# Performance work log

Hardware: AMD Instinct MI355X
Metric: run time of the kernel (lower is better)

Reference implementation:

```python
import jax, jax.numpy as jnp
import numpy as np

N, E, DIM, HEADS, EDIM, DFF = 20000, 320000, 256, 8, 32, 1024
C = DIM // HEADS


def _gatv2(x, src, dst, ea, Wl, Wr, We, att, b):
    # PyG GATv2Conv (concat=True, share_weights=False, add_self_loops=True,
    # fill_value='mean', negative_slope=0.2), eval mode (no attn dropout).
    n = x.shape[0]
    h, c = att.shape
    e = src.shape[0]
    # self loops: edge_attr filled with per-target-node mean of edge features
    cnt = jax.ops.segment_sum(jnp.ones((e,), x.dtype), dst, num_segments=n)
    loop_ea = jax.ops.segment_sum(ea, dst, num_segments=n) / jnp.maximum(cnt, 1.0)[:, None]
    loop = jnp.arange(n)
    s = jnp.concatenate([src, loop])
    d = jnp.concatenate([dst, loop])
    ea_all = jnp.concatenate([ea, loop_ea], axis=0)
    xl = (x @ Wl).reshape(n, h, c)   # source transform
    xr = (x @ Wr).reshape(n, h, c)   # target transform
    ee = (ea_all @ We).reshape(-1, h, c)
    z = jax.nn.leaky_relu(xl[s] + xr[d] + ee, 0.2)      # [E+N, H, C]
    score = jnp.einsum('ehc,hc->eh', z, att)             # [E+N, H]
    # segment softmax over incoming edges of each target node
    m = jax.ops.segment_max(score, d, num_segments=n)
    ex = jnp.exp(score - m[d])
    den = jax.ops.segment_sum(ex, d, num_segments=n)
    alpha = ex / den[d]
    out = jax.ops.segment_sum(alpha[:, :, None] * xl[s], d, num_segments=n)
    return out.reshape(n, h * c) + b


def _bn(x, g, b, eps=1e-5):
    # BatchNorm1d over nodes, training-mode batch stats (biased var)
    mu = x.mean(axis=0)
    var = ((x - mu) ** 2).mean(axis=0)
    return (x - mu) * jax.lax.rsqrt(var + eps) * g + b


def _lrelu(x):
    return jax.nn.leaky_relu(x, 0.01)  # F.leaky_relu default slope


def setup_inputs() -> dict:
    key = jax.random.key(0)
    ks = jax.random.split(key, 16)
    sc = 0.05
    inp = {
        'nf': jax.random.normal(ks[0], (N, DIM), jnp.float32),
        'ei': jax.random.randint(ks[1], (2, E), 0, N, dtype=jnp.int32),
        'ew': jax.random.normal(ks[2], (E, EDIM), jnp.float32),
    }
    for i, pfx in enumerate(['g1', 'g2']):
        kk = jax.random.split(ks[3 + i], 5)
        inp[pfx + '_Wl'] = jax.random.normal(kk[0], (DIM, DIM), jnp.float32) * sc
        inp[pfx + '_Wr'] = jax.random.normal(kk[1], (DIM, DIM), jnp.float32) * sc
        inp[pfx + '_We'] = jax.random.normal(kk[2], (EDIM, DIM), jnp.float32) * sc
        inp[pfx + '_att'] = jax.random.normal(kk[3], (HEADS, C), jnp.float32) * sc
        inp[pfx + '_b'] = jnp.zeros((DIM,), jnp.float32)
    for i, pfx in enumerate(['n1', 'n2', 'n3']):
        inp[pfx + '_g'] = jnp.ones((DIM,), jnp.float32)
        inp[pfx + '_b'] = jnp.zeros((DIM,), jnp.float32)
    inp['ff_W1'] = jax.random.normal(ks[8], (DIM, DFF), jnp.float32) * sc
    inp['ff_b1'] = jnp.zeros((DFF,), jnp.float32)
    inp['ff_W2'] = jax.random.normal(ks[9], (DFF, DIM), jnp.float32) * sc
    inp['ff_b2'] = jnp.zeros((DIM,), jnp.float32)
    return inp


def reference(nf, ei, ew,
              g1_Wl, g1_Wr, g1_We, g1_att, g1_b,
              g2_Wl, g2_Wr, g2_We, g2_att, g2_b,
              n1_g, n1_b, n2_g, n2_b, n3_g, n3_b,
              ff_W1, ff_b1, ff_W2, ff_b2):
    src, dst = ei[0], ei[1]
    # in_channels == dim, so residual branch is taken for block 1
    h = nf + _lrelu(_bn(_gatv2(nf, src, dst, ew, g1_Wl, g1_Wr, g1_We, g1_att, g1_b), n1_g, n1_b))
    h = h + _lrelu(_bn(_gatv2(h, src, dst, ew, g2_Wl, g2_Wr, g2_We, g2_att, g2_b), n2_g, n2_b))
    ff = jax.nn.relu(h @ ff_W1 + ff_b1) @ ff_W2 + ff_b2
    h = h + _lrelu(_bn(ff, n3_g, n3_b))
    return h
```

## Files before the change

### kernel.cpp

```cpp
#include <hip/hip_runtime.h>

#define NN 20000
#define NE 320000
#define DIMX 256
#define NHEADS 8
#define HC 32
#define EDIMX 32
#define DFFX 1024
#define TOT (NE + NN)
#define NGROUPS (TOT / 16)

using f32x4 = __attribute__((ext_vector_type(4))) float;
using bfrag = __attribute__((ext_vector_type(8))) short;

__device__ __forceinline__ float b2f(unsigned short u) {
  return __uint_as_float(((unsigned)u) << 16);
}
__device__ __forceinline__ unsigned short f2b(float f) {
  unsigned u = __float_as_uint(f);
  u += 0x7FFF + ((u >> 16) & 1);
  return (unsigned short)(u >> 16);
}

__global__ void k_detect(const unsigned short* __restrict__ in, int* __restrict__ flag) {
  __shared__ int cnt_s;
  if (threadIdx.x == 0) cnt_s = 0;
  __syncthreads();
  int c = 0;
  for (int i = threadIdx.x; i < 4096; i += 256) {
    int ex = (in[i] >> 7) & 0xFF;
    if (ex >= 0xC6) c++;
  }
  atomicAdd(&cnt_s, c);
  __syncthreads();
  if (threadIdx.x == 0) flag[0] = (cnt_s > 64) ? 1 : 0;
}

__global__ void k_cvt(const void* __restrict__ in, float* __restrict__ out, int n,
                      const int* __restrict__ flag) {
  int i = blockIdx.x * 256 + threadIdx.x;
  if (i >= n) return;
  if (flag[0]) out[i] = ((const float*)in)[i];
  else out[i] = b2f(((const unsigned short*)in)[i]);
}

__global__ void k_cvt_dual(const void* __restrict__ in, float* __restrict__ outf,
                           unsigned short* __restrict__ outb, int n,
                           const int* __restrict__ flag) {
  int i = blockIdx.x * 256 + threadIdx.x;
  if (i >= n) return;
  if (flag[0]) {
    float v = ((const float*)in)[i];
    outf[i] = v;
    outb[i] = f2b(v);
  } else {
    unsigned short u = ((const unsigned short*)in)[i];
    outf[i] = b2f(u);
    outb[i] = u;
  }
}

struct CvtArgs {
  const void* src[20];
  float* dst[20];
  int n[20];
};
__global__ void k_cvt_multi(CvtArgs a, const int* __restrict__ flag) {
  int seg = blockIdx.y;
  int n = a.n[seg];
  int i = blockIdx.x * 256 + threadIdx.x;
  if (i >= n) return;
  if (flag[0]) a.dst[seg][i] = ((const float*)a.src[seg])[i];
  else a.dst[seg][i] = b2f(((const unsigned short*)a.src[seg])[i]);
}

__global__ __launch_bounds__(256) void k_transpose(const float* __restrict__ in,
                                                   unsigned short* __restrict__ out,
                                                   int K, int N) {
  __shared__ float t[32][33];
  int n0 = blockIdx.x * 32, k0 = blockIdx.y * 32;
  int tx = threadIdx.x & 31, ty = threadIdx.x >> 5;
#pragma unroll
  for (int i = 0; i < 4; i++)
    t[ty + i * 8][tx] = in[(size_t)(k0 + ty + i * 8) * N + n0 + tx];
  __syncthreads();
#pragma unroll
  for (int i = 0; i < 4; i++)
    out[(size_t)(n0 + ty + i * 8) * K + k0 + tx] = f2b(t[tx][ty + i * 8]);
}

__global__ void k_edge_count(const int* __restrict__ dst, int* __restrict__ cnt, int E) {
  int e = blockIdx.x * 256 + threadIdx.x;
  if (e >= E) return;
  atomicAdd(&cnt[dst[e]], 1);
}

__global__ void k_scan(const int* __restrict__ cnt, int* __restrict__ rowptr, int N) {
  __shared__ int sums[256];
  int t = threadIdx.x;
  int chunk = (N + 255) / 256;
  int lo = t * chunk, hi = lo + chunk;
  if (hi > N) hi = N;
  if (lo > N) lo = N;
  int s = 0;
  for (int n = lo; n < hi; n++) s += cnt[n] + 1;
  sums[t] = s;
  __syncthreads();
  for (int off = 1; off < 256; off <<= 1) {
    int v = (t >= off) ? sums[t - off] : 0;
    __syncthreads();
    sums[t] += v;
    __syncthreads();
  }
  int run = sums[t] - s;
  for (int n = lo; n < hi; n++) { rowptr[n] = run; run += cnt[n] + 1; }
  if (t == 255) rowptr[N] = run;
}

__global__ void k_fill(const int* __restrict__ dst, const int* __restrict__ rowptr,
                       int* __restrict__ fill, int* __restrict__ eidx,
                       int* __restrict__ dstp, int N, int E) {
  int t = blockIdx.x * 256 + threadIdx.x;
  if (t < E) {
    int d = dst[t];
    int pos = rowptr[d] + atomicAdd(&fill[d], 1);
    eidx[pos] = t;
    dstp[pos] = d;
  } else if (t < E + N) {
    int n = t - E;
    int pos = rowptr[n + 1] - 1;
    eidx[pos] = E + n;
    dstp[pos] = n;
  }
}

__global__ __launch_bounds__(256) void k_lea(const float* __restrict__ ew,
                                             const int* __restrict__ rowptr,
                                             const int* __restrict__ eidx,
                                             float* __restrict__ lea, int N) {
  int wave = threadIdx.x >> 6, lane = threadIdx.x & 63;
  int node = blockIdx.x * 4 + wave;
  if (node >= N) return;
  int begin = rowptr[node], end = rowptr[node + 1] - 1;
  int ch = lane & 31, half = lane >> 5;
  float s = 0.f;
  for (int p = begin + half; p < end; p += 2) {
    int eid = eidx[p];
    s += ew[(size_t)eid * EDIMX + ch];
  }
  s += __shfl_xor(s, 32, 64);
  int deg = end - begin;
  if (lane < 32) lea[(size_t)node * EDIMX + ch] = s / (float)(deg > 0 ? deg : 1);
}

__global__ __launch_bounds__(256) void k_build_perm(const int* __restrict__ eidx,
                                                    const int* __restrict__ src,
                                                    const float* __restrict__ ewf,
                                                    const float* __restrict__ lea,
                                                    int* __restrict__ srcp,
                                                    unsigned short* __restrict__ eab,
                                                    int total, int E) {
  int g = blockIdx.x * 8 + (threadIdx.x >> 5);
  int lane = threadIdx.x & 31;
  if (g >= total) return;
  int eid = eidx[g];
  int s;
  const float* row;
  if (eid < E) {
    s = src[eid];
    row = ewf + (size_t)eid * EDIMX;
  } else {
    s = eid - E;
    row = lea + (size_t)(eid - E) * EDIMX;
  }
  if (lane == 0) srcp[g] = s;
  eab[(size_t)g * EDIMX + lane] = f2b(row[lane]);
}

template <bool BIAS, bool RELU, bool OUTBF16>
__global__ __launch_bounds__(256) void k_gemm_mfma(const unsigned short* __restrict__ A,
                                                   const unsigned short* __restrict__ BT,
                                                   const float* __restrict__ bias,
                                                   void* __restrict__ C, int M, int K, int N) {
  int tid = threadIdx.x;
  int wave = tid >> 6, lane = tid & 63;
  int quad = lane >> 4, l16 = lane & 15;
  int m0 = blockIdx.x * 64 + (wave & 1) * 32;
  int n0 = blockIdx.y * 64 + (wave >> 1) * 32;
  int mA0 = m0 + l16;
  if (mA0 > M - 1) mA0 = M - 1;
  int mA1 = m0 + 16 + l16;
  if (mA1 > M - 1) mA1 = M - 1;
  const bfrag* a0p = (const bfrag*)(A + (size_t)mA0 * K + quad * 8);
  const bfrag* a1p = (const bfrag*)(A + (size_t)mA1 * K + quad * 8);
  const bfrag* b0p = (const bfrag*)(BT + (size_t)(n0 + l16) * K + quad * 8);
  const bfrag* b1p = (const bfrag*)(BT + (size_t)(n0 + 16 + l16) * K + quad * 8);
  f32x4 acc00 = {0.f, 0.f, 0.f, 0.f}, acc01 = {0.f, 0.f, 0.f, 0.f};
  f32x4 acc10 = {0.f, 0.f, 0.f, 0.f}, acc11 = {0.f, 0.f, 0.f, 0.f};
  int ksteps = K >> 5;
  for (int kk = 0; kk < ksteps; kk++) {
    bfrag a0 = a0p[kk * 4];
    bfrag a1 = a1p[kk * 4];
    bfrag b0 = b0p[kk * 4];
    bfrag b1 = b1p[kk * 4];
    acc00 = __builtin_amdgcn_mfma_f32_16x16x32_bf16(a0, b0, acc00, 0, 0, 0);
    acc01 = __builtin_amdgcn_mfma_f32_16x16x32_bf16(a0, b1, acc01, 0, 0, 0);
    acc10 = __builtin_amdgcn_mfma_f32_16x16x32_bf16(a1, b0, acc10, 0, 0, 0);
    acc11 = __builtin_amdgcn_mfma_f32_16x16x32_bf16(a1, b1, acc11, 0, 0, 0);
  }
  float bv0 = 0.f, bv1 = 0.f;
  if (BIAS) {
    bv0 = bias[n0 + l16];
    bv1 = bias[n0 + 16 + l16];
  }
  int col0 = n0 + l16, col1 = n0 + 16 + l16;
#pragma unroll
  for (int r = 0; r < 4; r++) {
    int row0 = m0 + quad * 4 + r;
    int row1 = m0 + 16 + quad * 4 + r;
    float v00 = acc00[r] + bv0, v01 = acc01[r] + bv1;
    float v10 = acc10[r] + bv0, v11 = acc11[r] + bv1;
    if (RELU) {
      v00 = fmaxf(v00, 0.f); v01 = fmaxf(v01, 0.f);
      v10 = fmaxf(v10, 0.f); v11 = fmaxf(v11, 0.f);
    }
    if (row0 < M) {
      if (OUTBF16) {
        ((unsigned short*)C)[(size_t)row0 * N + col0] = f2b(v00);
        ((unsigned short*)C)[(size_t)row0 * N + col1] = f2b(v01);
      } else {
        ((float*)C)[(size_t)row0 * N + col0] = v00;
        ((float*)C)[(size_t)row0 * N + col1] = v01;
      }
    }
    if (row1 < M) {
      if (OUTBF16) {
        ((unsigned short*)C)[(size_t)row1 * N + col0] = f2b(v10);
        ((unsigned short*)C)[(size_t)row1 * N + col1] = f2b(v11);
      } else {
        ((float*)C)[(size_t)row1 * N + col0] = v10;
        ((float*)C)[(size_t)row1 * N + col1] = v11;
      }
    }
  }
}

__global__ __launch_bounds__(256) void k_score_mfma(
    const unsigned short* __restrict__ xlb, const unsigned short* __restrict__ xrb,
    const unsigned short* __restrict__ eab, const int* __restrict__ srcp,
    const int* __restrict__ dstp, const unsigned short* __restrict__ WET,
    const float* __restrict__ att, float* __restrict__ score, int ngroups) {
  __shared__ unsigned short We_s[256 * 40];
  __shared__ unsigned short ee_s[4][16 * 260];
  {
    int tid = threadIdx.x;
#pragma unroll
    for (int j = 0; j < 8; j++)
      *(ushort4*)&We_s[tid * 40 + j * 4] = *(const ushort4*)(WET + tid * 32 + j * 4);
  }
  __syncthreads();
  int wave = threadIdx.x >> 6, lane = threadIdx.x & 63;
  int quad = lane >> 4, l16 = lane & 15;
  int g = blockIdx.x * 4 + wave;
  if (g >= ngroups) return;
  int pbase = g * 16;
  const bfrag ea = *(const bfrag*)(eab + ((size_t)(pbase + l16) << 5) + quad * 8);
  f32x4 zero4 = {0.f, 0.f, 0.f, 0.f};
  f32x4 acc[16];
#pragma unroll
  for (int t = 0; t < 16; t++) {
    bfrag bw = *(const bfrag*)&We_s[(t * 16 + l16) * 40 + quad * 8];
    acc[t] = __builtin_amdgcn_mfma_f32_16x16x32_bf16(ea, bw, zero4, 0, 0, 0);
  }
#pragma unroll
  for (int t = 0; t < 16; t++) {
#pragma unroll
    for (int r = 0; r < 4; r++)
      ee_s[wave][(quad * 4 + r) * 260 + t * 16 + l16] = f2b(acc[t][r]);
  }
  int c0 = lane * 4;
  float4 a4 = *(const float4*)(att + c0);
  for (int e = 0; e < 16; e += 2) {
    int p0 = pbase + e, p1 = pbase + e + 1;
    int s0 = srcp[p0], d0 = dstp[p0];
    int s1 = srcp[p1], d1 = dstp[p1];
    ushort4 vl0 = *(const ushort4*)(xlb + ((size_t)s0 << 8) + c0);
    ushort4 vr0 = *(const ushort4*)(xrb + ((size_t)d0 << 8) + c0);
    ushort4 vl1 = *(const ushort4*)(xlb + ((size_t)s1 << 8) + c0);
    ushort4 vr1 = *(const ushort4*)(xrb + ((size_t)d1 << 8) + c0);
    ushort4 eu0 = *(const ushort4*)&ee_s[wave][e * 260 + c0];
    ushort4 eu1 = *(const ushort4*)&ee_s[wave][(e + 1) * 260 + c0];
    float z00 = b2f(vl0.x) + b2f(vr0.x) + b2f(eu0.x);
    float z01 = b2f(vl0.y) + b2f(vr0.y) + b2f(eu0.y);
    float z02 = b2f(vl0.z) + b2f(vr0.z) + b2f(eu0.z);
    float z03 = b2f(vl0.w) + b2f(vr0.w) + b2f(eu0.w);
    float z10 = b2f(vl1.x) + b2f(vr1.x) + b2f(eu1.x);
    float z11 = b2f(vl1.y) + b2f(vr1.y) + b2f(eu1.y);
    float z12 = b2f(vl1.z) + b2f(vr1.z) + b2f(eu1.z);
    float z13 = b2f(vl1.w) + b2f(vr1.w) + b2f(eu1.w);
    z00 = z00 > 0.f ? z00 : 0.2f * z00; z01 = z01 > 0.f ? z01 : 0.2f * z01;
    z02 = z02 > 0.f ? z02 : 0.2f * z02; z03 = z03 > 0.f ? z03 : 0.2f * z03;
    z10 = z10 > 0.f ? z10 : 0.2f * z10; z11 = z11 > 0.f ? z11 : 0.2f * z11;
    z12 = z12 > 0.f ? z12 : 0.2f * z12; z13 = z13 > 0.f ? z13 : 0.2f * z13;
    float sc0 = z00 * a4.x + z01 * a4.y + z02 * a4.z + z03 * a4.w;
    float sc1 = z10 * a4.x + z11 * a4.y + z12 * a4.z + z13 * a4.w;
    sc0 += __shfl_xor(sc0, 1, 64);
    sc1 += __shfl_xor(sc1, 1, 64);
    sc0 += __shfl_xor(sc0, 2, 64);
    sc1 += __shfl_xor(sc1, 2, 64);
    sc0 += __shfl_xor(sc0, 4, 64);
    sc1 += __shfl_xor(sc1, 4, 64);
    if ((lane & 7) == 0) {
      int h = lane >> 3;
      score[(size_t)p0 * 8 + h] = sc0;
      score[(size_t)p1 * 8 + h] = sc1;
    }
  }
}

__global__ __launch_bounds__(256) void k_agg(const unsigned short* __restrict__ xlb,
                                             const float* __restrict__ score,
                                             const int* __restrict__ srcp,
                                             const float* __restrict__ bias,
                                             const int* __restrict__ rowptr,
                                             float* __restrict__ out, int N) {
  int wave = threadIdx.x >> 6, lane = threadIdx.x & 63;
  int node = blockIdx.x * 4 + wave;
  if (node >= N) return;
  int begin = rowptr[node], end = rowptr[node + 1];
  int head = lane >> 3, sl = lane & 7;
  float m = -3.4e38f;
  for (int p = begin + sl; p < end; p += 8)
    m = fmaxf(m, score[(size_t)p * 8 + head]);
  m = fmaxf(m, __shfl_xor(m, 1, 64));
  m = fmaxf(m, __shfl_xor(m, 2, 64));
  m = fmaxf(m, __shfl_xor(m, 4, 64));
  float ssum = 0.f;
  for (int p = begin + sl; p < end; p += 8)
    ssum += __expf(score[(size_t)p * 8 + head] - m);
  ssum += __shfl_xor(ssum, 1, 64);
  ssum += __shfl_xor(ssum, 2, 64);
  ssum += __shfl_xor(ssum, 4, 64);
  float linv = 1.f / ssum;
  int c0 = lane * 4;
  float ax = 0.f, ay = 0.f, az = 0.f, aw = 0.f;
  for (int p = begin; p < end; p += 4) {
    int e1 = end - 1;
    int q1 = (p + 1 < end) ? p + 1 : e1;
    int q2 = (p + 2 < end) ? p + 2 : e1;
    int q3 = (p + 3 < end) ? p + 3 : e1;
    int s0 = srcp[p], s1 = srcp[q1], s2 = srcp[q2], s3 = srcp[q3];
    float sc0 = score[(size_t)p * 8 + head];
    float sc1 = score[(size_t)q1 * 8 + head];
    float sc2 = score[(size_t)q2 * 8 + head];
    float sc3 = score[(size_t)q3 * 8 + head];
    ushort4 v0 = *(const ushort4*)(xlb + ((size_t)s0 << 8) + c0);
    ushort4 v1 = *(const ushort4*)(xlb + ((size_t)s1 << 8) + c0);
    ushort4 v2 = *(const ushort4*)(xlb + ((size_t)s2 << 8) + c0);
    ushort4 v3 = *(const ushort4*)(xlb + ((size_t)s3 << 8) + c0);
    float w0 = __expf(sc0 - m) * linv;
    float w1 = (p + 1 < end) ? __expf(sc1 - m) * linv : 0.f;
    float w2 = (p + 2 < end) ? __expf(sc2 - m) * linv : 0.f;
    float w3 = (p + 3 < end) ? __expf(sc3 - m) * linv : 0.f;
    ax += w0 * b2f(v0.x) + w1 * b2f(v1.x) + w2 * b2f(v2.x) + w3 * b2f(v3.x);
    ay += w0 * b2f(v0.y) + w1 * b2f(v1.y) + w2 * b2f(v2.y) + w3 * b2f(v3.y);
    az += w0 * b2f(v0.z) + w1 * b2f(v1.z) + w2 * b2f(v2.z) + w3 * b2f(v3.z);
    aw += w0 * b2f(v0.w) + w1 * b2f(v1.w) + w2 * b2f(v2.w) + w3 * b2f(v3.w);
  }
  float4 bia = *(const float4*)(bias + c0);
  float4 acc = make_float4(ax + bia.x, ay + bia.y, az + bia.z, aw + bia.w);
  ((float4*)out)[(size_t)node * 64 + lane] = acc;
}

__global__ __launch_bounds__(256) void k_bnstats(const float* __restrict__ x,
                                                 float* __restrict__ sums, int N) {
  int c = threadIdx.x;
  float s = 0.f, sq = 0.f;
  for (int n = blockIdx.x; n < N; n += gridDim.x) {
    float v = x[(size_t)n * DIMX + c];
    s += v; sq += v * v;
  }
  atomicAdd(&sums[c], s);
  atomicAdd(&sums[DIMX + c], sq);
}

template <bool FINAL>
__global__ __launch_bounds__(256) void k_bnapply(const float* __restrict__ x,
                                                 const float* __restrict__ res,
                                                 const float* __restrict__ sums,
                                                 const float* __restrict__ g,
                                                 const float* __restrict__ b,
                                                 void* __restrict__ out,
                                                 unsigned short* __restrict__ outb, int N,
                                                 const int* __restrict__ flag) {
  int i = blockIdx.x * 256 + threadIdx.x;
  if (i >= N * DIMX) return;
  int c = i & (DIMX - 1);
  float invn = 1.f / (float)N;
  float mu = sums[c] * invn;
  float var = sums[DIMX + c] * invn - mu * mu;
  float rstd = rsqrtf(var + 1e-5f);
  float y = (x[i] - mu) * rstd * g[c] + b[c];
  y = y > 0.f ? y : 0.01f * y;
  y += res[i];
  if (FINAL) {
    if (flag[0]) ((float*)out)[i] = y;
    else ((unsigned short*)out)[i] = f2b(y);
  } else {
    ((float*)out)[i] = y;
    outb[i] = f2b(y);
  }
}

extern "C" void kernel_launch(void* const* d_in, const int* in_sizes, int n_in,
                              void* d_out, int out_size, void* d_ws, size_t ws_size,
                              hipStream_t stream) {
  (void)in_sizes; (void)n_in; (void)out_size; (void)ws_size;
  const int* ei = (const int*)d_in[1];
  const int* srcp = ei;
  const int* dstp = ei + NE;

  char* w = (char*)d_ws;
  auto alloc = [&](size_t bytes) {
    char* p = w;
    w += (bytes + 255) & ~(size_t)255;
    return p;
  };
  float* H0 = (float*)alloc((size_t)NN * DIMX * 4);
  float* H1 = (float*)alloc((size_t)NN * DIMX * 4);
  float* G = (float*)alloc((size_t)NN * DIMX * 4);
  float* LEA = (float*)alloc((size_t)NN * EDIMX * 4);
  float* EWF = (float*)alloc((size_t)NE * EDIMX * 4);
  float* PAR = (float*)alloc((size_t)806656 * 4);
  float* SCORE = (float*)alloc((size_t)TOT * NHEADS * 4);
  int* CNT = (int*)alloc((size_t)NN * 4);
  int* ROWPTR = (int*)alloc((size_t)(NN + 1) * 4);
  int* FILL = (int*)alloc((size_t)NN * 4);
  int* EIDX = (int*)alloc((size_t)TOT * 4);
  int* SRCP = (int*)alloc((size_t)TOT * 4);
  int* DSTP = (int*)alloc((size_t)TOT * 4);
  float* BNS = (float*)alloc(2 * DIMX * 4);
  int* FLAG = (int*)alloc(256);
  unsigned short* H0b = (unsigned short*)alloc((size_t)NN * DIMX * 2);
  unsigned short* H1b = (unsigned short*)alloc((size_t)NN * DIMX * 2);
  unsigned short* XLb = (unsigned short*)alloc((size_t)NN * DIMX * 2);
  unsigned short* XRb = (unsigned short*)alloc((size_t)NN * DIMX * 2);
  unsigned short* EAB = (unsigned short*)alloc((size_t)TOT * EDIMX * 2);
  unsigned short* WLT0 = (unsigned short*)alloc((size_t)DIMX * DIMX * 2);
  unsigned short* WRT0 = (unsigned short*)alloc((size_t)DIMX * DIMX * 2);
  unsigned short* WLT1 = (unsigned short*)alloc((size_t)DIMX * DIMX * 2);
  unsigned short* WRT1 = (unsigned short*)alloc((size_t)DIMX * DIMX * 2);
  unsigned short* WET0 = (unsigned short*)alloc((size_t)DIMX * EDIMX * 2);
  unsigned short* WET1 = (unsigned short*)alloc((size_t)DIMX * EDIMX * 2);
  unsigned short* W1T = (unsigned short*)alloc((size_t)DIMX * DFFX * 2);
  unsigned short* W2T = (unsigned short*)alloc((size_t)DFFX * DIMX * 2);
  unsigned short* FF1b = (unsigned short*)EWF;

  k_detect<<<1, 256, 0, stream>>>((const unsigned short*)d_in[0], FLAG);
  k_cvt_dual<<<(NN * DIMX + 255) / 256, 256, 0, stream>>>(d_in[0], H0, H0b, NN * DIMX, FLAG);
  k_cvt<<<(NE * EDIMX + 255) / 256, 256, 0, stream>>>(d_in[2], EWF, NE * EDIMX, FLAG);
  static const int psz[20] = {65536, 65536, 8192, 256, 256,
                              65536, 65536, 8192, 256, 256,
                              256, 256, 256, 256, 256, 256,
                              262144, 1024, 262144, 256};
  float* pp[20];
  {
    CvtArgs ca;
    int off = 0;
    for (int i = 0; i < 20; i++) {
      pp[i] = PAR + off;
      off += psz[i];
      ca.src[i] = d_in[3 + i];
      ca.dst[i] = pp[i];
      ca.n[i] = psz[i];
    }
    k_cvt_multi<<<dim3(262144 / 256, 20), 256, 0, stream>>>(ca, FLAG);
  }
  const float* g_att[2] = {pp[3], pp[8]};
  const float* g_b[2] = {pp[4], pp[9]};
  const float* bn_g[3] = {pp[10], pp[12], pp[14]};
  const float* bn_b[3] = {pp[11], pp[13], pp[15]};
  const float* ff_b1 = pp[17];
  const float* ff_b2 = pp[19];

  k_transpose<<<dim3(8, 8), 256, 0, stream>>>(pp[0], WLT0, DIMX, DIMX);
  k_transpose<<<dim3(8, 8), 256, 0, stream>>>(pp[1], WRT0, DIMX, DIMX);
  k_transpose<<<dim3(8, 8), 256, 0, stream>>>(pp[5], WLT1, DIMX, DIMX);
  k_transpose<<<dim3(8, 8), 256, 0, stream>>>(pp[6], WRT1, DIMX, DIMX);
  k_transpose<<<dim3(8, 1), 256, 0, stream>>>(pp[2], WET0, EDIMX, DIMX);
  k_transpose<<<dim3(8, 1), 256, 0, stream>>>(pp[7], WET1, EDIMX, DIMX);
  k_transpose<<<dim3(32, 8), 256, 0, stream>>>(pp[16], W1T, DIMX, DFFX);
  k_transpose<<<dim3(8, 32), 256, 0, stream>>>(pp[18], W2T, DFFX, DIMX);
  const unsigned short* WLT[2] = {WLT0, WLT1};
  const unsigned short* WRT[2] = {WRT0, WRT1};
  const unsigned short* WET[2] = {WET0, WET1};

  hipMemsetAsync(CNT, 0, (size_t)NN * 4, stream);
  hipMemsetAsync(FILL, 0, (size_t)NN * 4, stream);
  k_edge_count<<<(NE + 255) / 256, 256, 0, stream>>>(dstp, CNT, NE);
  k_scan<<<1, 256, 0, stream>>>(CNT, ROWPTR, NN);
  k_fill<<<(TOT + 255) / 256, 256, 0, stream>>>(dstp, ROWPTR, FILL, EIDX, DSTP, NN, NE);
  k_lea<<<(NN + 3) / 4, 256, 0, stream>>>(EWF, ROWPTR, EIDX, LEA, NN);
  k_build_perm<<<(TOT + 7) / 8, 256, 0, stream>>>(EIDX, srcp, EWF, LEA, SRCP, EAB, TOT, NE);

  const int MB = (NN + 63) / 64;
  auto run_gat = [&](const float* x, const unsigned short* xb, int li, int bi, float* hout,
                     unsigned short* houtb) {
    k_gemm_mfma<false, false, true><<<dim3(MB, 4), 256, 0, stream>>>(xb, WLT[li], nullptr, XLb,
                                                                     NN, DIMX, DIMX);
    k_gemm_mfma<false, false, true><<<dim3(MB, 4), 256, 0, stream>>>(xb, WRT[li], nullptr, XRb,
                                                                     NN, DIMX, DIMX);
    k_score_mfma<<<(NGROUPS + 3) / 4, 256, 0, stream>>>(XLb, XRb, EAB, SRCP, DSTP, WET[li],
                                                        g_att[li], SCORE, NGROUPS);
    k_agg<<<(NN + 3) / 4, 256, 0, stream>>>(XLb, SCORE, SRCP, g_b[li], ROWPTR, G, NN);
    hipMemsetAsync(BNS, 0, 2 * DIMX * 4, stream);
    k_bnstats<<<128, 256, 0, stream>>>(G, BNS, NN);
    k_bnapply<false><<<(NN * DIMX + 255) / 256, 256, 0, stream>>>(G, x, BNS, bn_g[bi], bn_b[bi],
                                                                  hout, houtb, NN, FLAG);
  };

  run_gat(H0, H0b, 0, 0, H1, H1b);
  run_gat(H1, H1b, 1, 1, H0, H0b);

  k_gemm_mfma<true, true, true><<<dim3(MB, DFFX / 64), 256, 0, stream>>>(H0b, W1T, ff_b1, FF1b,
                                                                         NN, DIMX, DFFX);
  k_gemm_mfma<true, false, false><<<dim3(MB, 4), 256, 0, stream>>>(FF1b, W2T, ff_b2, G, NN,
                                                                   DFFX, DIMX);
  hipMemsetAsync(BNS, 0, 2 * DIMX * 4, stream);
  k_bnstats<<<128, 256, 0, stream>>>(G, BNS, NN);
  k_bnapply<true><<<(NN * DIMX + 255) / 256, 256, 0, stream>>>(G, H0, BNS, bn_g[2], bn_b[2],
                                                               d_out, nullptr, NN, FLAG);
}
```

Before: 912.9 us.

## Fuse Wl/Wr GEMMs into one interleaved output, drop edge-feature conversion pass

Concatenates the transposed Wl and Wr weights so one GEMM writes an interleaved [N,512] buffer holding xl and xr per node. The score and aggregation kernels now index that buffer with a 512 stride. The separate fp32 conversion of edge features is removed, and k_lea and k_build_perm read the raw input directly with the dtype flag. The GEMM gains an NT template parameter so each block loops over several 64-column tiles while reusing its A row pointers; this cuts the number of blocks, which may lower occupancy and parallelism.

New measurement: 950.6 us. 4.1% more time.

```diff
diff --git a/kernel.cpp b/kernel.cpp
--- a/kernel.cpp
+++ b/kernel.cpp
@@ -34,14 +34,6 @@
   atomicAdd(&cnt_s, c);
   __syncthreads();
   if (threadIdx.x == 0) flag[0] = (cnt_s > 64) ? 1 : 0;
-}
-
-__global__ void k_cvt(const void* __restrict__ in, float* __restrict__ out, int n,
-                      const int* __restrict__ flag) {
-  int i = blockIdx.x * 256 + threadIdx.x;
-  if (i >= n) return;
-  if (flag[0]) out[i] = ((const float*)in)[i];
-  else out[i] = b2f(((const unsigned short*)in)[i]);
 }
 
 __global__ void k_cvt_dual(const void* __restrict__ in, float* __restrict__ outf,
@@ -134,10 +126,12 @@
   }
 }
 
-__global__ __launch_bounds__(256) void k_lea(const float* __restrict__ ew,
+__global__ __launch_bounds__(256) void k_lea(const void* __restrict__ ew,
                                              const int* __restrict__ rowptr,
                                              const int* __restrict__ eidx,
-                                             float* __restrict__ lea, int N) {
+                                             float* __restrict__ lea, int N,
+                                             const int* __restrict__ flag) {
+  int f = flag[0];
   int wave = threadIdx.x >> 6, lane = threadIdx.x & 63;
   int node = blockIdx.x * 4 + wave;
   if (node >= N) return;
@@ -146,7 +140,8 @@
   float s = 0.f;
   for (int p = begin + half; p < end; p += 2) {
     int eid = eidx[p];
-    s += ew[(size_t)eid * EDIMX + ch];
+    size_t idx = (size_t)eid * EDIMX + ch;
+    s += f ? ((const float*)ew)[idx] : b2f(((const unsigned short*)ew)[idx]);
   }
   s += __shfl_xor(s, 32, 64);
   int deg = end - begin;
@@ -155,29 +150,32 @@
 
 __global__ __launch_bounds__(256) void k_build_perm(const int* __restrict__ eidx,
                                                     const int* __restrict__ src,
-                                                    const float* __restrict__ ewf,
+                                                    const void* __restrict__ ew,
                                                     const float* __restrict__ lea,
                                                     int* __restrict__ srcp,
                                                     unsigned short* __restrict__ eab,
-                                                    int total, int E) {
+                                                    int total, int E,
+                                                    const int* __restrict__ flag) {
+  int f = flag[0];
   int g = blockIdx.x * 8 + (threadIdx.x >> 5);
   int lane = threadIdx.x & 31;
   if (g >= total) return;
   int eid = eidx[g];
+  unsigned short v;
   int s;
-  const float* row;
   if (eid < E) {
     s = src[eid];
-    row = ewf + (size_t)eid * EDIMX;
+    size_t idx = (size_t)eid * EDIMX + lane;
+    v = f ? f2b(((const float*)ew)[idx]) : ((const unsigned short*)ew)[idx];
   } else {
     s = eid - E;
-    row = lea + (size_t)(eid - E) * EDIMX;
+    v = f2b(lea[(size_t)(eid - E) * EDIMX + lane]);
   }
   if (lane == 0) srcp[g] = s;
-  eab[(size_t)g * EDIMX + lane] = f2b(row[lane]);
-}
-
-template <bool BIAS, bool RELU, bool OUTBF16>
+  eab[(size_t)g * EDIMX + lane] = v;
+}
+
+template <bool BIAS, bool RELU, bool OUTBF16, int NT>
 __global__ __launch_bounds__(256) void k_gemm_mfma(const unsigned short* __restrict__ A,
                                                    const unsigned short* __restrict__ BT,
                                                    const float* __restrict__ bias,
@@ -186,70 +184,73 @@
   int wave = tid >> 6, lane = tid & 63;
   int quad = lane >> 4, l16 = lane & 15;
   int m0 = blockIdx.x * 64 + (wave & 1) * 32;
-  int n0 = blockIdx.y * 64 + (wave >> 1) * 32;
   int mA0 = m0 + l16;
   if (mA0 > M - 1) mA0 = M - 1;
   int mA1 = m0 + 16 + l16;
   if (mA1 > M - 1) mA1 = M - 1;
   const bfrag* a0p = (const bfrag*)(A + (size_t)mA0 * K + quad * 8);
   const bfrag* a1p = (const bfrag*)(A + (size_t)mA1 * K + quad * 8);
-  const bfrag* b0p = (const bfrag*)(BT + (size_t)(n0 + l16) * K + quad * 8);
-  const bfrag* b1p = (const bfrag*)(BT + (size_t)(n0 + 16 + l16) * K + quad * 8);
-  f32x4 acc00 = {0.f, 0.f, 0.f, 0.f}, acc01 = {0.f, 0.f, 0.f, 0.f};
-  f32x4 acc10 = {0.f, 0.f, 0.f, 0.f}, acc11 = {0.f, 0.f, 0.f, 0.f};
   int ksteps = K >> 5;
-  for (int kk = 0; kk < ksteps; kk++) {
-    bfrag a0 = a0p[kk * 4];
-    bfrag a1 = a1p[kk * 4];
-    bfrag b0 = b0p[kk * 4];
-    bfrag b1 = b1p[kk * 4];
-    acc00 = __builtin_amdgcn_mfma_f32_16x16x32_bf16(a0, b0, acc00, 0, 0, 0);
-    acc01 = __builtin_amdgcn_mfma_f32_16x16x32_bf16(a0, b1, acc01, 0, 0, 0);
-    acc10 = __builtin_amdgcn_mfma_f32_16x16x32_bf16(a1, b0, acc10, 0, 0, 0);
-    acc11 = __builtin_amdgcn_mfma_f32_16x16x32_bf16(a1, b1, acc11, 0, 0, 0);
-  }
-  float bv0 = 0.f, bv1 = 0.f;
-  if (BIAS) {
-    bv0 = bias[n0 + l16];
-    bv1 = bias[n0 + 16 + l16];
-  }
-  int col0 = n0 + l16, col1 = n0 + 16 + l16;
-#pragma unroll
-  for (int r = 0; r < 4; r++) {
-    int row0 = m0 + quad * 4 + r;
-    int row1 = m0 + 16 + quad * 4 + r;
-    float v00 = acc00[r] + bv0, v01 = acc01[r] + bv1;
-    float v10 = acc10[r] + bv0, v11 = acc11[r] + bv1;
-    if (RELU) {
-      v00 = fmaxf(v00, 0.f); v01 = fmaxf(v01, 0.f);
-      v10 = fmaxf(v10, 0.f); v11 = fmaxf(v11, 0.f);
+#pragma unroll
+  for (int j = 0; j < NT; j++) {
+    int n0 = (blockIdx.y * NT + j) * 64 + (wave >> 1) * 32;
+    const bfrag* b0p = (const bfrag*)(BT + (size_t)(n0 + l16) * K + quad * 8);
+    const bfrag* b1p = (const bfrag*)(BT + (size_t)(n0 + 16 + l16) * K + quad * 8);
+    f32x4 acc00 = {0.f, 0.f, 0.f, 0.f}, acc01 = {0.f, 0.f, 0.f, 0.f};
+    f32x4 acc10 = {0.f, 0.f, 0.f, 0.f}, acc11 = {0.f, 0.f, 0.f, 0.f};
+    for (int kk = 0; kk < ksteps; kk++) {
+      bfrag a0 = a0p[kk * 4];
+      bfrag a1 = a1p[kk * 4];
+      bfrag b0 = b0p[kk * 4];
+      bfrag b1 = b1p[kk * 4];
+      acc00 = __builtin_amdgcn_mfma_f32_16x16x32_bf16(a0, b0, acc00, 0, 0, 0);
+      acc01 = __builtin_amdgcn_mfma_f32_16x16x32_bf16(a0, b1, acc01, 0, 0, 0);
+      acc10 = __builtin_amdgcn_mfma_f32_16x16x32_bf16(a1, b0, acc10, 0, 0, 0);
+      acc11 = __builtin_amdgcn_mfma_f32_16x16x32_bf16(a1, b1, acc11, 0, 0, 0);
     }
-    if (row0 < M) {
-      if (OUTBF16) {
-        ((unsigned short*)C)[(size_t)row0 * N + col0] = f2b(v00);
-        ((unsigned short*)C)[(size_t)row0 * N + col1] = f2b(v01);
-      } else {
-        ((float*)C)[(size_t)row0 * N + col0] = v00;
-        ((float*)C)[(size_t)row0 * N + col1] = v01;
+    float bv0 = 0.f, bv1 = 0.f;
+    if (BIAS) {
+      bv0 = bias[n0 + l16];
+      bv1 = bias[n0 + 16 + l16];
+    }
+    int col0 = n0 + l16, col1 = n0 + 16 + l16;
+#pragma unroll
+    for (int r = 0; r < 4; r++) {
+      int row0 = m0 + quad * 4 + r;
+      int row1 = m0 + 16 + quad * 4 + r;
+      float v00 = acc00[r] + bv0, v01 = acc01[r] + bv1;
+      float v10 = acc10[r] + bv0, v11 = acc11[r] + bv1;
+      if (RELU) {
+        v00 = fmaxf(v00, 0.f); v01 = fmaxf(v01, 0.f);
+        v10 = fmaxf(v10, 0.f); v11 = fmaxf(v11, 0.f);
+      }
+      if (row0 < M) {
+        if (OUTBF16) {
+          ((unsigned short*)C)[(size_t)row0 * N + col0] = f2b(v00);
+          ((unsigned short*)C)[(size_t)row0 * N + col1] = f2b(v01);
+        } else {
+          ((float*)C)[(size_t)row0 * N + col0] = v00;
+          ((float*)C)[(size_t)row0 * N + col1] = v01;
+        }
+      }
+      if (row1 < M) {
+        if (OUTBF16) {
+          ((unsigned short*)C)[(size_t)row1 * N + col0] = f2b(v10);
+          ((unsigned short*)C)[(size_t)row1 * N + col1] = f2b(v11);
+        } else {
+          ((float*)C)[(size_t)row1 * N + col0] = v10;
+          ((float*)C)[(size_t)row1 * N + col1] = v11;
+        }
       }
     }
-    if (row1 < M) {
-      if (OUTBF16) {
-        ((unsigned short*)C)[(size_t)row1 * N + col0] = f2b(v10);
-        ((unsigned short*)C)[(size_t)row1 * N + col1] = f2b(v11);
-      } else {
-        ((float*)C)[(size_t)row1 * N + col0] = v10;
-        ((float*)C)[(size_t)row1 * N + col1] = v11;
-      }
-    }
   }
 }
 
 __global__ __launch_bounds__(256) void k_score_mfma(
-    const unsigned short* __restrict__ xlb, const unsigned short* __restrict__ xrb,
-    const unsigned short* __restrict__ eab, const int* __restrict__ srcp,
-    const int* __restrict__ dstp, const unsigned short* __restrict__ WET,
-    const float* __restrict__ att, float* __restrict__ score, int ngroups) {
+    const unsigned short* __restrict__ xlr, const unsigned short* __restrict__ eab,
+    const int* __restrict__ srcp, const int* __restrict__ dstp,
+    const unsigned short* __restrict__ WET, const float* __restrict__ att,
+    float* __restrict__ score, int ngroups) {
   __shared__ unsigned short We_s[256 * 40];
   __shared__ unsigned short ee_s[4][16 * 260];
   {
@@ -284,10 +285,10 @@
     int p0 = pbase + e, p1 = pbase + e + 1;
     int s0 = srcp[p0], d0 = dstp[p0];
     int s1 = srcp[p1], d1 = dstp[p1];
-    ushort4 vl0 = *(const ushort4*)(xlb + ((size_t)s0 << 8) + c0);
-    ushort4 vr0 = *(const ushort4*)(xrb + ((size_t)d0 << 8) + c0);
-    ushort4 vl1 = *(const ushort4*)(xlb + ((size_t)s1 << 8) + c0);
-    ushort4 vr1 = *(const ushort4*)(xrb + ((size_t)d1 << 8) + c0);
+    ushort4 vl0 = *(const ushort4*)(xlr + ((size_t)s0 << 9) + c0);
+    ushort4 vr0 = *(const ushort4*)(xlr + ((size_t)d0 << 9) + 256 + c0);
+    ushort4 vl1 = *(const ushort4*)(xlr + ((size_t)s1 << 9) + c0);
+    ushort4 vr1 = *(const ushort4*)(xlr + ((size_t)d1 << 9) + 256 + c0);
     ushort4 eu0 = *(const ushort4*)&ee_s[wave][e * 260 + c0];
     ushort4 eu1 = *(const ushort4*)&ee_s[wave][(e + 1) * 260 + c0];
     float z00 = b2f(vl0.x) + b2f(vr0.x) + b2f(eu0.x);
@@ -318,7 +319,7 @@
   }
 }
 
-__global__ __launch_bounds__(256) void k_agg(const unsigned short* __restrict__ xlb,
+__global__ __launch_bounds__(256) void k_agg(const unsigned short* __restrict__ xlr,
                                              const float* __restrict__ score,
                                              const int* __restrict__ srcp,
                                              const float* __restrict__ bias,
@@ -354,10 +355,10 @@
     float sc1 = score[(size_t)q1 * 8 + head];
     float sc2 = score[(size_t)q2 * 8 + head];
     float sc3 = score[(size_t)q3 * 8 + head];
-    ushort4 v0 = *(const ushort4*)(xlb + ((size_t)s0 << 8) + c0);
-    ushort4 v1 = *(const ushort4*)(xlb + ((size_t)s1 << 8) + c0);
-    ushort4 v2 = *(const ushort4*)(xlb + ((size_t)s2 << 8) + c0);
-    ushort4 v3 = *(const ushort4*)(xlb + ((size_t)s3 << 8) + c0);
+    ushort4 v0 = *(const ushort4*)(xlr + ((size_t)s0 << 9) + c0);
+    ushort4 v1 = *(const ushort4*)(xlr + ((size_t)s1 << 9) + c0);
+    ushort4 v2 = *(const ushort4*)(xlr + ((size_t)s2 << 9) + c0);
+    ushort4 v3 = *(const ushort4*)(xlr + ((size_t)s3 << 9) + c0);
     float w0 = __expf(sc0 - m) * linv;
     float w1 = (p + 1 < end) ? __expf(sc1 - m) * linv : 0.f;
     float w2 = (p + 2 < end) ? __expf(sc2 - m) * linv : 0.f;
@@ -443,13 +444,10 @@
   int* FLAG = (int*)alloc(256);
   unsigned short* H0b = (unsigned short*)alloc((size_t)NN * DIMX * 2);
   unsigned short* H1b = (unsigned short*)alloc((size_t)NN * DIMX * 2);
-  unsigned short* XLb = (unsigned short*)alloc((size_t)NN * DIMX * 2);
-  unsigned short* XRb = (unsigned short*)alloc((size_t)NN * DIMX * 2);
+  unsigned short* XLRb = (unsigned short*)alloc((size_t)NN * 512 * 2);
   unsigned short* EAB = (unsigned short*)alloc((size_t)TOT * EDIMX * 2);
-  unsigned short* WLT0 = (unsigned short*)alloc((size_t)DIMX * DIMX * 2);
-  unsigned short* WRT0 = (unsigned short*)alloc((size_t)DIMX * DIMX * 2);
-  unsigned short* WLT1 = (unsigned short*)alloc((size_t)DIMX * DIMX * 2);
-  unsigned short* WRT1 = (unsigned short*)alloc((size_t)DIMX * DIMX * 2);
+  unsigned short* WLRT0 = (unsigned short*)alloc((size_t)512 * DIMX * 2);
+  unsigned short* WLRT1 = (unsigned short*)alloc((size_t)512 * DIMX * 2);
   unsigned short* WET0 = (unsigned short*)alloc((size_t)DIMX * EDIMX * 2);
   unsigned short* WET1 = (unsigned short*)alloc((size_t)DIMX * EDIMX * 2);
   unsigned short* W1T = (unsigned short*)alloc((size_t)DIMX * DFFX * 2);
@@ -458,7 +456,6 @@
 
   k_detect<<<1, 256, 0, stream>>>((const unsigned short*)d_in[0], FLAG);
   k_cvt_dual<<<(NN * DIMX + 255) / 256, 256, 0, stream>>>(d_in[0], H0, H0b, NN * DIMX, FLAG);
-  k_cvt<<<(NE * EDIMX + 255) / 256, 256, 0, stream>>>(d_in[2], EWF, NE * EDIMX, FLAG);
   static const int psz[20] = {65536, 65536, 8192, 256, 256,
                               65536, 65536, 8192, 256, 256,
                               256, 256, 256, 256, 256, 256,
@@ -483,16 +480,15 @@
   const float* ff_b1 = pp[17];
   const float* ff_b2 = pp[19];
 
-  k_transpose<<<dim3(8, 8), 256, 0, stream>>>(pp[0], WLT0, DIMX, DIMX);
-  k_transpose<<<dim3(8, 8), 256, 0, stream>>>(pp[1], WRT0, DIMX, DIMX);
-  k_transpose<<<dim3(8, 8), 256, 0, stream>>>(pp[5], WLT1, DIMX, DIMX);
-  k_transpose<<<dim3(8, 8), 256, 0, stream>>>(pp[6], WRT1, DIMX, DIMX);
+  k_transpose<<<dim3(8, 8), 256, 0, stream>>>(pp[0], WLRT0, DIMX, DIMX);
+  k_transpose<<<dim3(8, 8), 256, 0, stream>>>(pp[1], WLRT0 + 256 * DIMX, DIMX, DIMX);
+  k_transpose<<<dim3(8, 8), 256, 0, stream>>>(pp[5], WLRT1, DIMX, DIMX);
+  k_transpose<<<dim3(8, 8), 256, 0, stream>>>(pp[6], WLRT1 + 256 * DIMX, DIMX, DIMX);
   k_transpose<<<dim3(8, 1), 256, 0, stream>>>(pp[2], WET0, EDIMX, DIMX);
   k_transpose<<<dim3(8, 1), 256, 0, stream>>>(pp[7], WET1, EDIMX, DIMX);
   k_transpose<<<dim3(32, 8), 256, 0, stream>>>(pp[16], W1T, DIMX, DFFX);
   k_transpose<<<dim3(8, 32), 256, 0, stream>>>(pp[18], W2T, DFFX, DIMX);
-  const unsigned short* WLT[2] = {WLT0, WLT1};
-  const unsigned short* WRT[2] = {WRT0, WRT1};
+  const unsigned short* WLRT[2] = {WLRT0, WLRT1};
   const unsigned short* WET[2] = {WET0, WET1};
 
   hipMemsetAsync(CNT, 0, (size_t)NN * 4, stream);
@@ -500,19 +496,18 @@
   k_edge_count<<<(NE + 255) / 256, 256, 0, stream>>>(dstp, CNT, NE);
   k_scan<<<1, 256, 0, stream>>>(CNT, ROWPTR, NN);
   k_fill<<<(TOT + 255) / 256, 256, 0, stream>>>(dstp, ROWPTR, FILL, EIDX, DSTP, NN, NE);
-  k_lea<<<(NN + 3) / 4, 256, 0, stream>>>(EWF, ROWPTR, EIDX, LEA, NN);
-  k_build_perm<<<(TOT + 7) / 8, 256, 0, stream>>>(EIDX, srcp, EWF, LEA, SRCP, EAB, TOT, NE);
+  k_lea<<<(NN + 3) / 4, 256, 0, stream>>>(d_in[2], ROWPTR, EIDX, LEA, NN, FLAG);
+  k_build_perm<<<(TOT + 7) / 8, 256, 0, stream>>>(EIDX, srcp, d_in[2], LEA, SRCP, EAB, TOT, NE,
+                                                  FLAG);
 
   const int MB = (NN + 63) / 64;
   auto run_gat = [&](const float* x, const unsigned short* xb, int li, int bi, float* hout,
                      unsigned short* houtb) {
-    k_gemm_mfma<false, false, true><<<dim3(MB, 4), 256, 0, stream>>>(xb, WLT[li], nullptr, XLb,
-                                                                     NN, DIMX, DIMX);
-    k_gemm_mfma<false, false, true><<<dim3(MB, 4), 256, 0, stream>>>(xb, WRT[li], nullptr, XRb,
-                                                                     NN, DIMX, DIMX);
-    k_score_mfma<<<(NGROUPS + 3) / 4, 256, 0, stream>>>(XLb, XRb, EAB, SRCP, DSTP, WET[li],
+    k_gemm_mfma<false, false, true, 4><<<dim3(MB, 2), 256, 0, stream>>>(xb, WLRT[li], nullptr,
+                                                                        XLRb, NN, DIMX, 512);
+    k_score_mfma<<<(NGROUPS + 3) / 4, 256, 0, stream>>>(XLRb, EAB, SRCP, DSTP, WET[li],
                                                         g_att[li], SCORE, NGROUPS);
-    k_agg<<<(NN + 3) / 4, 256, 0, stream>>>(XLb, SCORE, SRCP, g_b[li], ROWPTR, G, NN);
+    k_agg<<<(NN + 3) / 4, 256, 0, stream>>>(XLRb, SCORE, SRCP, g_b[li], ROWPTR, G, NN);
     hipMemsetAsync(BNS, 0, 2 * DIMX * 4, stream);
     k_bnstats<<<128, 256, 0, stream>>>(G, BNS, NN);
     k_bnapply<false><<<(NN * DIMX + 255) / 256, 256, 0, stream>>>(G, x, BNS, bn_g[bi], bn_b[bi],
@@ -522,10 +517,11 @@
   run_gat(H0, H0b, 0, 0, H1, H1b);
   run_gat(H1, H1b, 1, 1, H0, H0b);
 
-  k_gemm_mfma<true, true, true><<<dim3(MB, DFFX / 64), 256, 0, stream>>>(H0b, W1T, ff_b1, FF1b,
-                                                                         NN, DIMX, DFFX);
-  k_gemm_mfma<true, false, false><<<dim3(MB, 4), 256, 0, stream>>>(FF1b, W2T, ff_b2, G, NN,
-                                                                   DFFX, DIMX);
+  k_gemm_mfma<true, true, true, 4><<<dim3(MB, DFFX / 256), 256, 0, stream>>>(H0b, W1T, ff_b1,
+                                                                             FF1b, NN, DIMX,
+                                                                             DFFX);
+  k_gemm_mfma<true, false, false, 4><<<dim3(MB, 1), 256, 0, stream>>>(FF1b, W2T, ff_b2, G, NN,
+                                                                      DFFX, DIMX);
   hipMemsetAsync(BNS, 0, 2 * DIMX * 4, stream);
   k_bnstats<<<128, 256, 0, stream>>>(G, BNS, NN);
   k_bnapply<true><<<(NN * DIMX + 255) / 256, 256, 0, stream>>>(G, H0, BNS, bn_g[2], bn_b[2],
```
